# Kernel tuning notes

Hardware: AMD Instinct MI355X
Metric: run time of the kernel (lower is better)

## Reference

```python
import jax, jax.numpy as jnp
import numpy as np
from jax import lax

B, T, C, H, W = 2, 64, 32, 64, 64   # (batch, feat-channels t, bands c, height, width)
NH = 4                              # num_heads; head dim = C//NH
HID = int(T * 2.66)                 # GDFN hidden channels = 170
EPS_LN = 1e-5
EPS_L2 = 1e-12


def _dwconv3d(x, w, pad):
    # x: (B, Cg, D, H, W); w: (Cg, 1, kd, kh, kw) depthwise
    cg = x.shape[1]
    return lax.conv_general_dilated(
        x, w, window_strides=(1, 1, 1), padding=pad,
        dimension_numbers=('NCDHW', 'OIDHW', 'NCDHW'),
        feature_group_count=cg)


def _pw(w, x):
    # 1x1x1 conv == channel GEMM; w: (out, in)
    return jnp.einsum('oi,bidhw->bodhw', w, x)


def _ln_ch(x, g, b):
    # LayerNorm over channel dim (dim1), matching reshape/transpose dance in torch
    m = jnp.mean(x, axis=1, keepdims=True)
    v = jnp.var(x, axis=1, keepdims=True)
    xn = (x - m) * lax.rsqrt(v + EPS_LN)
    return xn * g[None, :, None, None, None] + b[None, :, None, None, None]


def _attn(x, temperature, qkv_w, qkv_dw, attn_out_w):
    b, t, c, h, w = x.shape
    qkv = _dwconv3d(_pw(qkv_w, x), qkv_dw, ((0, 0), (1, 1), (1, 1)))  # (b,3t,c,h,w)
    q, k, v = jnp.split(qkv, 3, axis=1)
    L = h * w * t
    X = (t * c * h * w) // (NH * L)  # == c // NH
    rsh = lambda a: a.reshape(b, NH, X, L)
    q, k, v = rsh(q), rsh(k), rsh(v)
    l2n = lambda a: a / jnp.maximum(jnp.linalg.norm(a, axis=-1, keepdims=True), EPS_L2)
    q, k = l2n(q), l2n(k)
    scores = jnp.einsum('bnxl,bnyl->bnxy', q, k) * temperature  # (b,NH,X,X)
    att = jax.nn.softmax(scores, axis=-1)
    o = jnp.einsum('bnxy,bnyl->bnxl', att, v).reshape(b, t, c, h, w)
    return _pw(attn_out_w, o)


def _ffn(x, pin_w, dw_w, pout_w):
    y = _dwconv3d(_pw(pin_w, x), dw_w, ((1, 1), (1, 1), (1, 1)))  # (b,2*HID,c,h,w)
    x1, x2 = jnp.split(y, 2, axis=1)
    return _pw(pout_w, jax.nn.gelu(x1, approximate=False) * x2)


def setup_inputs() -> dict:
    key = jax.random.key(0)
    ks = jax.random.split(key, 12)
    s = lambda *sh: 1.0 / np.sqrt(np.prod(sh[1:]) if len(sh) > 1 else 1.0)
    p = lambda k, *sh: jax.random.normal(k, sh, dtype=jnp.float32) * s(*sh)
    return {
        'x': jax.random.normal(ks[0], (B, T, C, H, W), dtype=jnp.float32),
        'norm1_g': jnp.ones((T,), jnp.float32),
        'norm1_b': jnp.zeros((T,), jnp.float32),
        'temperature': jnp.ones((1, NH, 1, 1), jnp.float32),
        'qkv_w': p(ks[1], 3 * T, T),
        'qkv_dw': p(ks[2], 3 * T, 1, 1, 3, 3),
        'attn_out_w': p(ks[3], T, T),
        'norm2_g': jnp.ones((T,), jnp.float32),
        'norm2_b': jnp.zeros((T,), jnp.float32),
        'pin_w': p(ks[4], 2 * HID, T),
        'dw_w': p(ks[5], 2 * HID, 1, 3, 3, 3),
        'pout_w': p(ks[6], T, HID),
        'se_w': p(ks[7], T, T),
        'se_b': jnp.zeros((T,), jnp.float32),
    }


def reference(x, norm1_g, norm1_b, temperature, qkv_w, qkv_dw, attn_out_w,
              norm2_g, norm2_b, pin_w, dw_w, pout_w, se_w, se_b):
    x = x + _attn(_ln_ch(x, norm1_g, norm1_b), temperature, qkv_w, qkv_dw, attn_out_w)
    x = x + _ffn(_ln_ch(x, norm2_g, norm2_b), pin_w, dw_w, pout_w)
    s = jnp.mean(x, axis=(2, 3, 4), keepdims=True)               # GlobalAvgPool3d
    s = jax.nn.sigmoid(_pw(se_w, s) + se_b[None, :, None, None, None])
    return s * x
```

## Files before the change

kernel.cpp:

```cpp
#include <hip/hip_runtime.h>
#include <hip/hip_bf16.h>
#include <math.h>

typedef __hip_bfloat16 bf16;

#define S_ 131072

#define OFF_QKVW 0
#define OFF_AOW  12288
#define OFF_PINW 16384
#define OFF_POUTW 38912
#define OFF_SEW  49792
#define OFF_QDW  53888
#define OFF_DWW  55616
#define OFF_N1G  64796
#define OFF_N1B  64860
#define OFF_N2G  64924
#define OFF_N2B  64988
#define OFF_SEB  65052
#define OFF_TEMP 65116
#define WB_TOTAL 65120

#define SM_SSQ 0
#define SM_SSK 64
#define SM_ATT 128
#define SM_MEAN 640
#define SM_SVEC 768
#define SM_M 896
#define SM_FLAGI 9216

#define WSOFF_SM 262144
#define WSOFF_X1 303104
#define WSOFF_R  33857536
#define WS_REQUIRED 134520832ull

#define NCHUNK 256

__device__ __forceinline__ float toF(float v) { return v; }
__device__ __forceinline__ float toF(bf16 v) { return __bfloat162float(v); }

__device__ __forceinline__ float bfbitsToF(unsigned short u) {
  union { unsigned int i; float f; } x;
  x.i = ((unsigned int)u) << 16;
  return x.f;
}

__device__ __forceinline__ unsigned short bfBits(float f) {
  bf16 h = __float2bfloat16(f);
  return *reinterpret_cast<unsigned short*>(&h);
}

__device__ __forceinline__ float ldIn(const void* p, size_t i, int isbf) {
  return isbf ? __bfloat162float(((const bf16*)p)[i]) : ((const float*)p)[i];
}
__device__ __forceinline__ void stOut(void* p, size_t i, int isbf, float v) {
  if (isbf) ((bf16*)p)[i] = __float2bfloat16(v);
  else ((float*)p)[i] = v;
}

__device__ __forceinline__ float wred(float v) {
#pragma unroll
  for (int o = 32; o > 0; o >>= 1) v += __shfl_down(v, o, 64);
  return v;
}

__device__ __forceinline__ float conv9(const bf16* __restrict__ plane,
                                       const float* __restrict__ wp, int h, int w) {
  float a = 0.f;
#pragma unroll
  for (int dh = -1; dh <= 1; ++dh) {
    int hh = h + dh;
    if ((unsigned)hh >= 64u) continue;
#pragma unroll
    for (int dw = -1; dw <= 1; ++dw) {
      int ww = w + dw;
      if ((unsigned)ww >= 64u) continue;
      a = fmaf(toF(plane[hh * 64 + ww]), wp[(dh + 1) * 3 + (dw + 1)], a);
    }
  }
  return a;
}

__device__ __forceinline__ void conv4(const bf16* __restrict__ plane,
                                      const float* __restrict__ w9,
                                      int h, int w0, bool wlo, bool whi,
                                      float& o0, float& o1, float& o2, float& o3) {
  o0 = o1 = o2 = o3 = 0.f;
#pragma unroll
  for (int rr = 0; rr < 3; ++rr) {
    int hh = h - 1 + rr;
    if ((unsigned)hh < 64u) {
      const bf16* row = plane + hh * 64 + w0;
      ushort4 m = *reinterpret_cast<const ushort4*>(row);
      float v1 = bfbitsToF(m.x), v2 = bfbitsToF(m.y);
      float v3 = bfbitsToF(m.z), v4 = bfbitsToF(m.w);
      float v0 = wlo ? toF(row[-1]) : 0.f;
      float v5 = whi ? toF(row[4]) : 0.f;
      float wa = w9[rr * 3 + 0], wbb = w9[rr * 3 + 1], wc = w9[rr * 3 + 2];
      o0 = fmaf(wa, v0, fmaf(wbb, v1, fmaf(wc, v2, o0)));
      o1 = fmaf(wa, v1, fmaf(wbb, v2, fmaf(wc, v3, o1)));
      o2 = fmaf(wa, v2, fmaf(wbb, v3, fmaf(wc, v4, o2)));
      o3 = fmaf(wa, v3, fmaf(wbb, v4, fmaf(wc, v5, o3)));
    }
  }
}

__global__ void zero_sm(float* sm, const unsigned* n1g_raw) {
  for (int i = threadIdx.x; i < 768; i += 256) sm[i] = 0.f;
  if (threadIdx.x == 0) {
    ((int*)sm)[SM_FLAGI] = ((n1g_raw[0] & 0xFFFFu) != 0u) ? 1 : 0;
  }
}

__global__ void convert_w(const void* qkvw, const void* aow, const void* pinw,
                          const void* poutw, const void* sew, const void* qdw,
                          const void* dww, const void* n1g, const void* n1b,
                          const void* n2g, const void* n2b, const void* seb,
                          const void* temp, float* wb, const int* dflag) {
  int i = blockIdx.x * 256 + threadIdx.x;
  if (i >= WB_TOTAL) return;
  int f = *dflag;
  float v;
  if (i < OFF_AOW) v = ldIn(qkvw, i, f);
  else if (i < OFF_PINW) v = ldIn(aow, i - OFF_AOW, f);
  else if (i < OFF_POUTW) { int r = i - OFF_PINW; v = (r < 21760) ? ldIn(pinw, r, f) : 0.f; }
  else if (i < OFF_SEW) v = ldIn(poutw, i - OFF_POUTW, f);
  else if (i < OFF_QDW) v = ldIn(sew, i - OFF_SEW, f);
  else if (i < OFF_DWW) v = ldIn(qdw, i - OFF_QDW, f);
  else if (i < OFF_N1G) v = ldIn(dww, i - OFF_DWW, f);
  else if (i < OFF_N1B) v = ldIn(n1g, i - OFF_N1G, f);
  else if (i < OFF_N2G) v = ldIn(n1b, i - OFF_N1B, f);
  else if (i < OFF_N2B) v = ldIn(n2g, i - OFF_N2G, f);
  else if (i < OFF_SEB) v = ldIn(n2b, i - OFF_N2B, f);
  else if (i < OFF_TEMP) v = ldIn(seb, i - OFF_SEB, f);
  else v = ldIn(temp, i - OFF_TEMP, f);
  wb[i] = v;
}

__global__ __launch_bounds__(256) void qkv_ln_gemm(const void* __restrict__ x,
                                                   const float* __restrict__ wb,
                                                   bf16* __restrict__ qraw,
                                                   const int* __restrict__ dflag) {
  int p = blockIdx.x * 256 + threadIdx.x;
  int b = p >> 17, s = p & (S_ - 1);
  int isbf = *dflag;
  size_t ibase = (size_t)b * 64 * S_ + s;
  float xin[64];
  if (isbf) {
    const bf16* xb = (const bf16*)x;
#pragma unroll
    for (int t = 0; t < 64; ++t) xin[t] = toF(xb[ibase + (size_t)t * S_]);
  } else {
    const float* xf = (const float*)x;
#pragma unroll
    for (int t = 0; t < 64; ++t) xin[t] = xf[ibase + (size_t)t * S_];
  }
  float sum = 0.f;
#pragma unroll
  for (int t = 0; t < 64; ++t) sum += xin[t];
  float mean = sum * (1.f / 64.f);
  float ss = 0.f;
#pragma unroll
  for (int t = 0; t < 64; ++t) { float d = xin[t] - mean; ss += d * d; }
  float rstd = rsqrtf(ss * (1.f / 64.f) + 1e-5f);
#pragma unroll
  for (int t = 0; t < 64; ++t)
    xin[t] = (xin[t] - mean) * rstd * wb[OFF_N1G + t] + wb[OFF_N1B + t];
  size_t obase = (size_t)b * 192 * S_ + s;
  for (int oc = 0; oc < 192; oc += 16) {
    float acc[16];
#pragma unroll
    for (int j = 0; j < 16; ++j) acc[j] = 0.f;
    const float* wp = wb + OFF_QKVW + oc * 64;
#pragma unroll
    for (int t = 0; t < 64; ++t) {
      float xv = xin[t];
#pragma unroll
      for (int j = 0; j < 16; ++j) acc[j] = fmaf(wp[j * 64 + t], xv, acc[j]);
    }
#pragma unroll
    for (int j = 0; j < 16; ++j)
      qraw[obase + (size_t)(oc + j) * S_] = __float2bfloat16(acc[j]);
  }
}

__global__ __launch_bounds__(256, 2) void attn_scores(const bf16* __restrict__ qraw,
                                                      const float* __restrict__ wb,
                                                      float* __restrict__ part) {
  int blk = blockIdx.x;
  int bh = blk >> 8, chunk = blk & (NCHUNK - 1);
  int b = bh >> 2, nh = bh & 3;
  int pbit = chunk >> 7;
  int c = (chunk >> 2) & 31;
  int hq = chunk & 3;
  int tid = threadIdx.x;
  int wseg = tid & 15, w0 = wseg * 4;
  int h = hq * 16 + (tid >> 4);
  bool wlo = (wseg != 0), whi = (wseg != 15);

  float dq[8], dk[8], dot[64], qv[8][4];
#pragma unroll
  for (int i = 0; i < 8; ++i) { dq[i] = 0.f; dk[i] = 0.f; }
#pragma unroll
  for (int i = 0; i < 64; ++i) dot[i] = 0.f;

  const size_t bbase = ((size_t)(b * 192)) << 17;

#pragma unroll
  for (int r = 0; r < 8; ++r) {
    int ch = 2 * (nh * 8 + r) + pbit;
    const bf16* pl = qraw + bbase + (((size_t)ch) << 17) + (c << 12);
    float o0, o1, o2, o3;
    conv4(pl, wb + OFF_QDW + ch * 9, h, w0, wlo, whi, o0, o1, o2, o3);
    qv[r][0] = o0; qv[r][1] = o1; qv[r][2] = o2; qv[r][3] = o3;
    dq[r] = fmaf(o0, o0, fmaf(o1, o1, fmaf(o2, o2, fmaf(o3, o3, dq[r]))));
  }
#pragma unroll
  for (int r = 0; r < 8; ++r) {
    int ch = 64 + 2 * (nh * 8 + r) + pbit;
    const bf16* pl = qraw + bbase + (((size_t)ch) << 17) + (c << 12);
    float k0, k1, k2, k3;
    conv4(pl, wb + OFF_QDW + ch * 9, h, w0, wlo, whi, k0, k1, k2, k3);
    dk[r] = fmaf(k0, k0, fmaf(k1, k1, fmaf(k2, k2, fmaf(k3, k3, dk[r]))));
#pragma unroll
    for (int i = 0; i < 8; ++i)
      dot[i * 8 + r] = fmaf(qv[i][0], k0, fmaf(qv[i][1], k1,
                       fmaf(qv[i][2], k2, fmaf(qv[i][3], k3, dot[i * 8 + r]))));
  }

  __shared__ float red[4][80];
  int lane = threadIdx.x & 63, wid = threadIdx.x >> 6;
#pragma unroll
  for (int i = 0; i < 8; ++i) {
    float v = wred(dq[i]);
    if (lane == 0) red[wid][i] = v;
    v = wred(dk[i]);
    if (lane == 0) red[wid][8 + i] = v;
  }
#pragma unroll
  for (int ij = 0; ij < 64; ++ij) {
    float v = wred(dot[ij]);
    if (lane == 0) red[wid][16 + ij] = v;
  }
  __syncthreads();
  if (threadIdx.x < 80)
    part[blk * 80 + threadIdx.x] = red[0][threadIdx.x] + red[1][threadIdx.x] +
                                   red[2][threadIdx.x] + red[3][threadIdx.x];
}

__global__ void attn_reduce(const float* __restrict__ part, float* __restrict__ sm) {
  int o = blockIdx.x;
  int bh = o / 80, v = o - bh * 80;
  __shared__ float s[256];
  s[threadIdx.x] = part[(bh * NCHUNK + threadIdx.x) * 80 + v];
  __syncthreads();
#pragma unroll
  for (int st = 128; st > 0; st >>= 1) {
    if (threadIdx.x < st) s[threadIdx.x] += s[threadIdx.x + st];
    __syncthreads();
  }
  if (threadIdx.x == 0) {
    float r = s[0];
    if (v < 8) sm[SM_SSQ + bh * 8 + v] = r;
    else if (v < 16) sm[SM_SSK + bh * 8 + (v - 8)] = r;
    else sm[SM_ATT + bh * 64 + (v - 16)] = r;
  }
}

__global__ void attn_softmax_m(float* __restrict__ sm, const float* __restrict__ wb) {
  int t = threadIdx.x;
  if (t < 64) {
    int bh = t >> 3, i = t & 7, nh = bh & 3;
    float invq = 1.f / fmaxf(sqrtf(sm[SM_SSQ + bh * 8 + i]), 1e-12f);
    float temp = wb[OFF_TEMP + nh];
    float sc[8];
#pragma unroll
    for (int j = 0; j < 8; ++j) {
      float invk = 1.f / fmaxf(sqrtf(sm[SM_SSK + bh * 8 + j]), 1e-12f);
      sc[j] = sm[SM_ATT + bh * 64 + i * 8 + j] * invq * invk * temp;
    }
    float mx = sc[0];
#pragma unroll
    for (int j = 1; j < 8; ++j) mx = fmaxf(mx, sc[j]);
    float sum = 0.f;
#pragma unroll
    for (int j = 0; j < 8; ++j) { sc[j] = expf(sc[j] - mx); sum += sc[j]; }
    float inv = 1.f / sum;
#pragma unroll
    for (int j = 0; j < 8; ++j) sm[SM_ATT + bh * 64 + i * 8 + j] = sc[j] * inv;
  }
  __syncthreads();
  for (int k = 0; k < 32; ++k) {
    int idx = t + k * 256;
    int b = idx >> 12;
    int rest = idx & 4095;
    int tout = rest >> 6, tv = rest & 63;
    int n = (tv >> 4) & 3, j = (tv >> 1) & 7, pbit = tv & 1;
    float acc = 0.f;
#pragma unroll
    for (int i = 0; i < 8; ++i)
      acc = fmaf(wb[OFF_AOW + tout * 64 + ((n * 8 + i) * 2 + pbit)],
                 sm[SM_ATT + (b * 4 + n) * 64 + i * 8 + j], acc);
    sm[SM_M + b * 4096 + tv * 64 + tout] = acc;
  }
}

__global__ __launch_bounds__(256) void attn_apply_out(const bf16* __restrict__ qraw,
                                                      const float* __restrict__ sm,
                                                      const float* __restrict__ wb,
                                                      const void* __restrict__ x,
                                                      bf16* __restrict__ x1,
                                                      const int* __restrict__ dflag) {
  int b = blockIdx.x >> 9;
  int ssp = ((blockIdx.x & 511) << 8) | threadIdx.x;
  int isbf = *dflag;
  int c = ssp >> 12, h = (ssp >> 6) & 63, w = ssp & 63;
  const float* Mg = sm + SM_M + b * 4096;
  float acc[64];
#pragma unroll
  for (int j = 0; j < 64; ++j) acc[j] = 0.f;
  const bf16* vbase = qraw + (((size_t)(b * 192 + 128)) << 17) + (c << 12);
  for (int tv = 0; tv < 64; ++tv) {
    float v = conv9(vbase + ((size_t)tv << 17), wb + OFF_QDW + (128 + tv) * 9, h, w);
    const float* mrow = Mg + tv * 64;
#pragma unroll
    for (int j = 0; j < 64; ++j) acc[j] = fmaf(mrow[j], v, acc[j]);
  }
  size_t obase = (size_t)b * 64 * S_ + ssp;
#pragma unroll
  for (int j = 0; j < 64; ++j) {
    size_t oi = obase + (size_t)j * S_;
    x1[oi] = __float2bfloat16(acc[j] + ldIn(x, oi, isbf));
  }
}

__global__ __launch_bounds__(256) void pin_ln_gemm(const bf16* __restrict__ x1,
                                                   const float* __restrict__ wb,
                                                   bf16* __restrict__ slab, int c0) {
  int p = blockIdx.x * 256 + threadIdx.x;
  int b = p >> 17, s = p & (S_ - 1);
  const bf16* xp = x1 + (size_t)b * 64 * S_ + s;
  float xin[64];
  float sum = 0.f;
#pragma unroll
  for (int t = 0; t < 64; ++t) { xin[t] = toF(xp[(size_t)t * S_]); sum += xin[t]; }
  float mean = sum * (1.f / 64.f);
  float ss = 0.f;
#pragma unroll
  for (int t = 0; t < 64; ++t) { float d = xin[t] - mean; ss += d * d; }
  float rstd = rsqrtf(ss * (1.f / 64.f) + 1e-5f);
#pragma unroll
  for (int t = 0; t < 64; ++t)
    xin[t] = (xin[t] - mean) * rstd * wb[OFF_N2G + t] + wb[OFF_N2B + t];
  size_t obase = (size_t)b * 64 * S_ + s;
  for (int jc = 0; jc < 4; ++jc) {
    float acc[16];
    int rows[16];
#pragma unroll
    for (int jj = 0; jj < 16; ++jj) {
      acc[jj] = 0.f;
      int j = jc * 16 + jj;
      int c1 = c0 + (j & 31);
      rows[jj] = (c1 < 170) ? (c1 + ((j >= 32) ? 170 : 0)) : 0;
    }
#pragma unroll
    for (int t = 0; t < 64; ++t) {
      float xv = xin[t];
#pragma unroll
      for (int jj = 0; jj < 16; ++jj)
        acc[jj] = fmaf(wb[OFF_PINW + rows[jj] * 64 + t], xv, acc[jj]);
    }
#pragma unroll
    for (int jj = 0; jj < 16; ++jj) {
      int j = jc * 16 + jj;
      if (c0 + (j & 31) < 170)
        slab[obase + (size_t)j * S_] = __float2bfloat16(acc[jj]);
    }
  }
}

__global__ __launch_bounds__(256) void dw3d_gelu_chunk(const bf16* __restrict__ slab,
                                                       const float* __restrict__ wb,
                                                       bf16* __restrict__ g,
                                                       int c0, int nch) {
  int blk = blockIdx.x;
  int hq = blk & 3, c = (blk >> 2) & 31;
  int r = blk >> 7;
  int lj = r % nch, b = r / nch;
  int c1 = c0 + lj;
  int tid = threadIdx.x;
  int wseg = tid & 15, w0 = wseg * 4;
  int h = hq * 16 + (tid >> 4);
  bool wlo = (wseg != 0), whi = (wseg != 15);
  const bf16* p1 = slab + (((size_t)(b * 64 + lj)) << 17);
  const bf16* p2 = slab + (((size_t)(b * 64 + 32 + lj)) << 17);
  const float* w1 = wb + OFF_DWW + c1 * 27;
  const float* w2 = wb + OFF_DWW + (c1 + 170) * 27;
  float a10 = 0.f, a11 = 0.f, a12 = 0.f, a13 = 0.f;
  float a20 = 0.f, a21 = 0.f, a22 = 0.f, a23 = 0.f;
#pragma unroll
  for (int dc = -1; dc <= 1; ++dc) {
    int cc = c + dc;
    if ((unsigned)cc >= 32u) continue;
    const bf16* q1 = p1 + ((size_t)cc << 12);
    const bf16* q2 = p2 + ((size_t)cc << 12);
    const float* u1 = w1 + (dc + 1) * 9;
    const float* u2 = w2 + (dc + 1) * 9;
#pragma unroll
    for (int rr = 0; rr < 3; ++rr) {
      int hh = h - 1 + rr;
      if ((unsigned)hh < 64u) {
        const bf16* r1 = q1 + hh * 64 + w0;
        const bf16* r2 = q2 + hh * 64 + w0;
        ushort4 m1 = *reinterpret_cast<const ushort4*>(r1);
        ushort4 m2 = *reinterpret_cast<const ushort4*>(r2);
        float p0 = wlo ? toF(r1[-1]) : 0.f;
        float p5 = whi ? toF(r1[4]) : 0.f;
        float s0 = wlo ? toF(r2[-1]) : 0.f;
        float s5 = whi ? toF(r2[4]) : 0.f;
        float pa = bfbitsToF(m1.x), pb = bfbitsToF(m1.y);
        float pc = bfbitsToF(m1.z), pd = bfbitsToF(m1.w);
        float sa = bfbitsToF(m2.x), sb = bfbitsToF(m2.y);
        float sc = bfbitsToF(m2.z), sd = bfbitsToF(m2.w);
        float wa = u1[rr * 3 + 0], wbv = u1[rr * 3 + 1], wc = u1[rr * 3 + 2];
        a10 = fmaf(wa, p0, fmaf(wbv, pa, fmaf(wc, pb, a10)));
        a11 = fmaf(wa, pa, fmaf(wbv, pb, fmaf(wc, pc, a11)));
        a12 = fmaf(wa, pb, fmaf(wbv, pc, fmaf(wc, pd, a12)));
        a13 = fmaf(wa, pc, fmaf(wbv, pd, fmaf(wc, p5, a13)));
        float xa = u2[rr * 3 + 0], xb = u2[rr * 3 + 1], xc = u2[rr * 3 + 2];
        a20 = fmaf(xa, s0, fmaf(xb, sa, fmaf(xc, sb, a20)));
        a21 = fmaf(xa, sa, fmaf(xb, sb, fmaf(xc, sc, a21)));
        a22 = fmaf(xa, sb, fmaf(xb, sc, fmaf(xc, sd, a22)));
        a23 = fmaf(xa, sc, fmaf(xb, sd, fmaf(xc, s5, a23)));
      }
    }
  }
  float ge0 = 0.5f * a10 * (1.f + erff(a10 * 0.70710678118f));
  float ge1 = 0.5f * a11 * (1.f + erff(a11 * 0.70710678118f));
  float ge2 = 0.5f * a12 * (1.f + erff(a12 * 0.70710678118f));
  float ge3 = 0.5f * a13 * (1.f + erff(a13 * 0.70710678118f));
  int sp = (c << 12) + (h << 6) + w0;
  bf16* dst = g + (((size_t)(b * 170 + c1)) << 17) + sp;
  ushort4 st;
  st.x = bfBits(ge0 * a20); st.y = bfBits(ge1 * a21);
  st.z = bfBits(ge2 * a22); st.w = bfBits(ge3 * a23);
  *reinterpret_cast<ushort4*>(dst) = st;
}

__global__ __launch_bounds__(256, 4) void pout_gemm(const bf16* __restrict__ g,
                                                    const float* __restrict__ wb,
                                                    const bf16* __restrict__ x1,
                                                    void* __restrict__ out,
                                                    const int* __restrict__ dflag) {
  int blk = blockIdx.x;
  int sblk = blk & 255, jh = (blk >> 8) & 1, b = blk >> 9;
  int s = (sblk << 9) | (threadIdx.x << 1);
  int isbf = *dflag;
  const bf16* ip = g + (size_t)b * 170 * S_ + s;
  const float* wp = wb + OFF_POUTW + (jh * 32) * 170;
  float a0[32], a1[32];
#pragma unroll
  for (int j = 0; j < 32; ++j) { a0[j] = 0.f; a1[j] = 0.f; }

  float cx[4], cy[4];
#pragma unroll
  for (int u = 0; u < 4; ++u) {
    ushort2 m = *reinterpret_cast<const ushort2*>(ip + (size_t)u * S_);
    cx[u] = bfbitsToF(m.x); cy[u] = bfbitsToF(m.y);
  }
  for (int t = 0; t < 168; t += 4) {
    float nx[4], ny[4];
#pragma unroll
    for (int u = 0; u < 4; ++u) {
      ushort2 m = *reinterpret_cast<const ushort2*>(ip + (size_t)(t + 4 + u) * S_);
      nx[u] = bfbitsToF(m.x); ny[u] = bfbitsToF(m.y);
    }
#pragma unroll
    for (int u = 0; u < 4; ++u) {
#pragma unroll
      for (int j = 0; j < 32; ++j) {
        float wv = wp[j * 170 + t + u];
        a0[j] = fmaf(wv, cx[u], a0[j]);
        a1[j] = fmaf(wv, cy[u], a1[j]);
      }
    }
#pragma unroll
    for (int u = 0; u < 4; ++u) { cx[u] = nx[u]; cy[u] = ny[u]; }
  }
#pragma unroll
  for (int u = 0; u < 2; ++u) {
#pragma unroll
    for (int j = 0; j < 32; ++j) {
      float wv = wp[j * 170 + 168 + u];
      a0[j] = fmaf(wv, cx[u], a0[j]);
      a1[j] = fmaf(wv, cy[u], a1[j]);
    }
  }

  size_t obase = (size_t)b * 64 * S_ + s;
#pragma unroll
  for (int j = 0; j < 32; ++j) {
    size_t oi = obase + (size_t)(jh * 32 + j) * S_;
    stOut(out, oi,     isbf, a0[j] + toF(x1[oi]));
    stOut(out, oi + 1, isbf, a1[j] + toF(x1[oi + 1]));
  }
}

__global__ __launch_bounds__(256) void se_mean(const void* __restrict__ xo,
                                               float* __restrict__ mean,
                                               const int* __restrict__ dflag) {
  int row = blockIdx.x >> 3;
  int part = blockIdx.x & 7;
  int isbf = *dflag;
  size_t base = (size_t)row * S_ + part * 16384;
  float s = 0.f;
  for (int i = threadIdx.x; i < 16384; i += 256) s += ldIn(xo, base + i, isbf);
  s = wred(s);
  __shared__ float red[4];
  int lane = threadIdx.x & 63, wid = threadIdx.x >> 6;
  if (lane == 0) red[wid] = s;
  __syncthreads();
  if (threadIdx.x == 0)
    atomicAdd(&mean[row], (red[0] + red[1] + red[2] + red[3]) * (1.f / S_));
}

__global__ void se_vec(const float* __restrict__ wb, float* __restrict__ sm) {
  int t = threadIdx.x;
  int b = t >> 6, o = t & 63;
  float acc = wb[OFF_SEB + o];
  for (int k = 0; k < 64; ++k)
    acc = fmaf(wb[OFF_SEW + o * 64 + k], sm[SM_MEAN + b * 64 + k], acc);
  sm[SM_SVEC + t] = 1.f / (1.f + expf(-acc));
}

__global__ __launch_bounds__(256) void se_scale(void* __restrict__ xo,
                                                const float* __restrict__ svec,
                                                const int* __restrict__ dflag) {
  size_t i = (size_t)blockIdx.x * 256 + threadIdx.x;
  int row = (int)(i >> 17);
  int isbf = *dflag;
  stOut(xo, i, isbf, ldIn(xo, i, isbf) * svec[row]);
}

extern "C" void kernel_launch(void* const* d_in, const int* in_sizes, int n_in,
                              void* d_out, int out_size, void* d_ws, size_t ws_size,
                              hipStream_t stream) {
  if (ws_size < WS_REQUIRED) return;

  char* ws = (char*)d_ws;
  float* WB  = (float*)ws;
  float* SM  = (float*)(ws + WSOFF_SM);
  const int* FLAG = (const int*)(SM + SM_FLAGI);
  bf16*  X1  = (bf16*)(ws + WSOFF_X1);
  float* PART= (float*)(ws + WSOFF_X1);
  bf16*  QR  = (bf16*)(ws + WSOFF_R);
  bf16*  G   = (bf16*)(ws + WSOFF_R);
  bf16*  SLAB= (bf16*)d_out;

  zero_sm<<<1, 256, 0, stream>>>(SM, (const unsigned*)d_in[1]);
  convert_w<<<(WB_TOTAL + 255) / 256, 256, 0, stream>>>(
      d_in[4], d_in[6], d_in[9], d_in[11], d_in[12], d_in[5], d_in[10],
      d_in[1], d_in[2], d_in[7], d_in[8], d_in[13], d_in[3], WB, FLAG);

  qkv_ln_gemm<<<1024, 256, 0, stream>>>(d_in[0], WB, QR, FLAG);
  attn_scores<<<8 * NCHUNK, 256, 0, stream>>>(QR, WB, PART);
  attn_reduce<<<640, 256, 0, stream>>>(PART, SM);
  attn_softmax_m<<<1, 256, 0, stream>>>(SM, WB);
  attn_apply_out<<<1024, 256, 0, stream>>>(QR, SM, WB, d_in[0], X1, FLAG);

  for (int c0 = 0; c0 < 170; c0 += 32) {
    int nch = (170 - c0 < 32) ? (170 - c0) : 32;
    pin_ln_gemm<<<1024, 256, 0, stream>>>(X1, WB, SLAB, c0);
    dw3d_gelu_chunk<<<nch * 256, 256, 0, stream>>>(SLAB, WB, G, c0, nch);
  }
  pout_gemm<<<1024, 256, 0, stream>>>(G, WB, X1, d_out, FLAG);

  se_mean<<<1024, 256, 0, stream>>>(d_out, SM + SM_MEAN, FLAG);
  se_vec<<<1, 128, 0, stream>>>(WB, SM);
  se_scale<<<65536, 256, 0, stream>>>(d_out, SM + SM_SVEC, FLAG);
}
```

Baseline: 1.503 ms.

## Split V depthwise conv out of attention apply and parallelize QKV GEMM halves

```diff
diff --git a/kernel.cpp b/kernel.cpp
--- a/kernel.cpp
+++ b/kernel.cpp
@@ -62,23 +62,6 @@
 #pragma unroll
   for (int o = 32; o > 0; o >>= 1) v += __shfl_down(v, o, 64);
   return v;
-}
-
-__device__ __forceinline__ float conv9(const bf16* __restrict__ plane,
-                                       const float* __restrict__ wp, int h, int w) {
-  float a = 0.f;
-#pragma unroll
-  for (int dh = -1; dh <= 1; ++dh) {
-    int hh = h + dh;
-    if ((unsigned)hh >= 64u) continue;
-#pragma unroll
-    for (int dw = -1; dw <= 1; ++dw) {
-      int ww = w + dw;
-      if ((unsigned)ww >= 64u) continue;
-      a = fmaf(toF(plane[hh * 64 + ww]), wp[(dh + 1) * 3 + (dw + 1)], a);
-    }
-  }
-  return a;
 }
 
 __device__ __forceinline__ void conv4(const bf16* __restrict__ plane,
@@ -141,7 +124,8 @@
                                                    const float* __restrict__ wb,
                                                    bf16* __restrict__ qraw,
                                                    const int* __restrict__ dflag) {
-  int p = blockIdx.x * 256 + threadIdx.x;
+  int oh = blockIdx.x >> 10;
+  int p = ((blockIdx.x & 1023) << 8) | threadIdx.x;
   int b = p >> 17, s = p & (S_ - 1);
   int isbf = *dflag;
   size_t ibase = (size_t)b * 64 * S_ + s;
@@ -167,7 +151,8 @@
   for (int t = 0; t < 64; ++t)
     xin[t] = (xin[t] - mean) * rstd * wb[OFF_N1G + t] + wb[OFF_N1B + t];
   size_t obase = (size_t)b * 192 * S_ + s;
-  for (int oc = 0; oc < 192; oc += 16) {
+  int oc0 = oh * 96;
+  for (int oc = oc0; oc < oc0 + 96; oc += 16) {
     float acc[16];
 #pragma unroll
     for (int j = 0; j < 16; ++j) acc[j] = 0.f;
@@ -267,6 +252,24 @@
   }
 }
 
+__global__ __launch_bounds__(256) void v_dwconv(const bf16* __restrict__ qraw,
+                                                const float* __restrict__ wb,
+                                                bf16* __restrict__ vc) {
+  int blk = blockIdx.x;
+  int hq = blk & 3, c = (blk >> 2) & 31, tv = (blk >> 7) & 63, b = blk >> 13;
+  int tid = threadIdx.x;
+  int wseg = tid & 15, w0 = wseg * 4;
+  int h = hq * 16 + (tid >> 4);
+  bool wlo = (wseg != 0), whi = (wseg != 15);
+  const bf16* pl = qraw + (((size_t)(b * 192 + 128 + tv)) << 17) + (c << 12);
+  float o0, o1, o2, o3;
+  conv4(pl, wb + OFF_QDW + (128 + tv) * 9, h, w0, wlo, whi, o0, o1, o2, o3);
+  bf16* dst = vc + (((size_t)(b * 64 + tv)) << 17) + (c << 12) + h * 64 + w0;
+  ushort4 st;
+  st.x = bfBits(o0); st.y = bfBits(o1); st.z = bfBits(o2); st.w = bfBits(o3);
+  *reinterpret_cast<ushort4*>(dst) = st;
+}
+
 __global__ void attn_softmax_m(float* __restrict__ sm, const float* __restrict__ wb) {
   int t = threadIdx.x;
   if (t < 64) {
@@ -305,32 +308,64 @@
   }
 }
 
-__global__ __launch_bounds__(256) void attn_apply_out(const bf16* __restrict__ qraw,
-                                                      const float* __restrict__ sm,
-                                                      const float* __restrict__ wb,
-                                                      const void* __restrict__ x,
-                                                      bf16* __restrict__ x1,
-                                                      const int* __restrict__ dflag) {
-  int b = blockIdx.x >> 9;
-  int ssp = ((blockIdx.x & 511) << 8) | threadIdx.x;
+__global__ __launch_bounds__(256, 4) void attn_apply_gemm(const bf16* __restrict__ vc,
+                                                          const float* __restrict__ sm,
+                                                          const void* __restrict__ x,
+                                                          bf16* __restrict__ x1,
+                                                          const int* __restrict__ dflag) {
+  int blk = blockIdx.x;
+  int sblk = blk & 255, jh = (blk >> 8) & 1, b = blk >> 9;
+  int s = (sblk << 9) | (threadIdx.x << 1);
   int isbf = *dflag;
-  int c = ssp >> 12, h = (ssp >> 6) & 63, w = ssp & 63;
-  const float* Mg = sm + SM_M + b * 4096;
-  float acc[64];
-#pragma unroll
-  for (int j = 0; j < 64; ++j) acc[j] = 0.f;
-  const bf16* vbase = qraw + (((size_t)(b * 192 + 128)) << 17) + (c << 12);
-  for (int tv = 0; tv < 64; ++tv) {
-    float v = conv9(vbase + ((size_t)tv << 17), wb + OFF_QDW + (128 + tv) * 9, h, w);
-    const float* mrow = Mg + tv * 64;
-#pragma unroll
-    for (int j = 0; j < 64; ++j) acc[j] = fmaf(mrow[j], v, acc[j]);
-  }
-  size_t obase = (size_t)b * 64 * S_ + ssp;
-#pragma unroll
-  for (int j = 0; j < 64; ++j) {
-    size_t oi = obase + (size_t)j * S_;
-    x1[oi] = __float2bfloat16(acc[j] + ldIn(x, oi, isbf));
+  const bf16* ip = vc + (((size_t)(b * 64)) << 17) + s;
+  const float* Mg = sm + SM_M + b * 4096 + jh * 32;
+  float a0[32], a1[32];
+#pragma unroll
+  for (int j = 0; j < 32; ++j) { a0[j] = 0.f; a1[j] = 0.f; }
+
+  float cx[4], cy[4];
+#pragma unroll
+  for (int u = 0; u < 4; ++u) {
+    ushort2 m = *reinterpret_cast<const ushort2*>(ip + (size_t)u * S_);
+    cx[u] = bfbitsToF(m.x); cy[u] = bfbitsToF(m.y);
+  }
+  for (int t = 0; t < 60; t += 4) {
+    float nx[4], ny[4];
+#pragma unroll
+    for (int u = 0; u < 4; ++u) {
+      ushort2 m = *reinterpret_cast<const ushort2*>(ip + (size_t)(t + 4 + u) * S_);
+      nx[u] = bfbitsToF(m.x); ny[u] = bfbitsToF(m.y);
+    }
+#pragma unroll
+    for (int u = 0; u < 4; ++u) {
+      const float* mrow = Mg + (t + u) * 64;
+#pragma unroll
+      for (int j = 0; j < 32; ++j) {
+        float wv = mrow[j];
+        a0[j] = fmaf(wv, cx[u], a0[j]);
+        a1[j] = fmaf(wv, cy[u], a1[j]);
+      }
+    }
+#pragma unroll
+    for (int u = 0; u < 4; ++u) { cx[u] = nx[u]; cy[u] = ny[u]; }
+  }
+#pragma unroll
+  for (int u = 0; u < 4; ++u) {
+    const float* mrow = Mg + (60 + u) * 64;
+#pragma unroll
+    for (int j = 0; j < 32; ++j) {
+      float wv = mrow[j];
+      a0[j] = fmaf(wv, cx[u], a0[j]);
+      a1[j] = fmaf(wv, cy[u], a1[j]);
+    }
+  }
+
+  size_t obase = (size_t)b * 64 * S_ + s;
+#pragma unroll
+  for (int j = 0; j < 32; ++j) {
+    size_t oi = obase + (size_t)(jh * 32 + j) * S_;
+    x1[oi]     = __float2bfloat16(a0[j] + ldIn(x, oi, isbf));
+    x1[oi + 1] = __float2bfloat16(a1[j] + ldIn(x, oi + 1, isbf));
   }
 }
 
@@ -556,17 +591,19 @@
   bf16*  QR  = (bf16*)(ws + WSOFF_R);
   bf16*  G   = (bf16*)(ws + WSOFF_R);
   bf16*  SLAB= (bf16*)d_out;
+  bf16*  VC  = (bf16*)d_out;
 
   zero_sm<<<1, 256, 0, stream>>>(SM, (const unsigned*)d_in[1]);
   convert_w<<<(WB_TOTAL + 255) / 256, 256, 0, stream>>>(
       d_in[4], d_in[6], d_in[9], d_in[11], d_in[12], d_in[5], d_in[10],
       d_in[1], d_in[2], d_in[7], d_in[8], d_in[13], d_in[3], WB, FLAG);
 
-  qkv_ln_gemm<<<1024, 256, 0, stream>>>(d_in[0], WB, QR, FLAG);
+  qkv_ln_gemm<<<2048, 256, 0, stream>>>(d_in[0], WB, QR, FLAG);
   attn_scores<<<8 * NCHUNK, 256, 0, stream>>>(QR, WB, PART);
   attn_reduce<<<640, 256, 0, stream>>>(PART, SM);
+  v_dwconv<<<16384, 256, 0, stream>>>(QR, WB, VC);
   attn_softmax_m<<<1, 256, 0, stream>>>(SM, WB);
-  attn_apply_out<<<1024, 256, 0, stream>>>(QR, SM, WB, d_in[0], X1, FLAG);
+  attn_apply_gemm<<<1024, 256, 0, stream>>>(VC, SM, d_in[0], X1, FLAG);
 
   for (int c0 = 0; c0 < 170; c0 += 32) {
     int nch = (170 - c0 < 32) ? (170 - c0) : 32;
```

Result: faster. 1.404 ms (-6.6%).
